# Kernel tuning notes

Hardware: AMD Instinct MI355X
Metric: run time of the kernel (lower is better)

The kernel has to match this reference:

```python
import jax, jax.numpy as jnp
import numpy as np

OBJ_DIM = 1024
NUM_REL_CLS = 8
N_OBJ = 4096
N_PAIRS = 65536


def setup_inputs() -> dict:
    key = jax.random.key(0)
    k1, k2, k3, k4, k5, k6 = jax.random.split(key, 6)
    obj_feats = jax.random.normal(k1, (N_OBJ, OBJ_DIM), dtype=jnp.float32)
    pairs = jax.random.randint(k2, (N_PAIRS, 2), 0, N_OBJ, dtype=jnp.int64)
    # proto_support_detector params: Linear(2*obj_dim -> obj_dim), Linear(obj_dim -> num_rel_cls)
    s1 = 1.0 / np.sqrt(2 * OBJ_DIM)
    s2 = 1.0 / np.sqrt(OBJ_DIM)
    W1 = jax.random.uniform(k3, (OBJ_DIM, 2 * OBJ_DIM), jnp.float32, -s1, s1)
    b1 = jax.random.uniform(k4, (OBJ_DIM,), jnp.float32, -s1, s1)
    W2 = jax.random.uniform(k5, (NUM_REL_CLS, OBJ_DIM), jnp.float32, -s2, s2)
    b2 = jax.random.uniform(k6, (NUM_REL_CLS,), jnp.float32, -s2, s2)
    return {"obj_feats": obj_feats, "pairs": pairs, "W1": W1, "b1": b1, "W2": W2, "b2": b2}


def reference(obj_feats, pairs, W1, b1, W2, b2):
    # Batched form of the per-pair proto_support_detector calls:
    #   rel_feat = Linear(cat([sub, obj], -1)); rel_dist = Linear(rel_feat)
    sub = obj_feats[pairs[:, 0]]                      # [P, D] gather
    obj = obj_feats[pairs[:, 1]]                      # [P, D] gather
    rel_feat = jnp.concatenate([sub, obj], axis=-1)   # [P, 2D]
    rel_feat = rel_feat @ W1.T + b1                   # [P, D]
    rel_dist = rel_feat @ W2.T + b2                   # [P, C]
    return rel_dist
```

## Files before the change

### kernel.cpp

```cpp
#include <hip/hip_runtime.h>

#define OBJ_DIM 1024
#define NREL 8
#define NOBJ 4096
#define NPAIRS 65536

#define WC_OFF   0
#define CVEC_OFF 16384
#define PROJ_OFF 16400

__global__ __launch_bounds__(256) void prep_kernel(
    const float* __restrict__ W1, const float* __restrict__ W2,
    const float* __restrict__ b1, float* __restrict__ Wc,
    float* __restrict__ cvec)
{
    const int cblk = blockIdx.x & 7;
    const int kblk = blockIdx.x >> 3;
    const int c  = cblk * 256 + threadIdx.x;
    const int k0 = kblk * 32;

    float acc[NREL];
#pragma unroll
    for (int r = 0; r < NREL; ++r) acc[r] = 0.f;

#pragma unroll 8
    for (int kk = 0; kk < 32; ++kk) {
        const int k = k0 + kk;
        const float w1 = W1[(size_t)k * 2048 + c];
#pragma unroll
        for (int r = 0; r < NREL; ++r)
            acc[r] += W2[r * 1024 + k] * w1;
    }
#pragma unroll
    for (int r = 0; r < NREL; ++r)
        atomicAdd(&Wc[r * 2048 + c], acc[r]);

    if (cblk == 0 && threadIdx.x < 32) {
        const int k = k0 + (int)threadIdx.x;
        const float bb = b1[k];
#pragma unroll
        for (int r = 0; r < NREL; ++r) {
            float v = W2[r * 1024 + k] * bb;
            v += __shfl_down(v, 16);
            v += __shfl_down(v, 8);
            v += __shfl_down(v, 4);
            v += __shfl_down(v, 2);
            v += __shfl_down(v, 1);
            if (threadIdx.x == 0) atomicAdd(&cvec[r], v);
        }
    }
}

__global__ __launch_bounds__(256) void proj_kernel(
    const float* __restrict__ obj, const float* __restrict__ Wc,
    float* __restrict__ proj)
{
    __shared__ float sh[16 * 1024];

    const int t = threadIdx.x;
#pragma unroll
    for (int i = 0; i < 16; ++i) {
        const int f4 = t + 256 * i;
        const int f  = f4 * 4;
        const int r   = f >> 11;
        const int rem = f & 2047;
        const int h   = rem >> 10;
        const int k   = rem & 1023;
        const float4 v = ((const float4*)Wc)[f4];
        *((float4*)&sh[(h * 8 + r) * 1024 + k]) = v;
    }
    __syncthreads();

    const int wave = t >> 6, lane = t & 63;
    const int n0 = blockIdx.x * 8 + wave * 2;
    const float4* xa = (const float4*)(obj + (size_t)n0 * 1024);
    const float4* xb = xa + 256;

    float4 x0[4], x1[4];
#pragma unroll
    for (int i = 0; i < 4; ++i) {
        x0[i] = xa[lane + 64 * i];
        x1[i] = xb[lane + 64 * i];
    }

    float a0[16], a1[16];
#pragma unroll
    for (int q = 0; q < 16; ++q) {
        float s0 = 0.f, s1 = 0.f;
        const float4* wq = (const float4*)(sh + q * 1024);
#pragma unroll
        for (int i = 0; i < 4; ++i) {
            const float4 w = wq[lane + 64 * i];
            s0 += w.x * x0[i].x + w.y * x0[i].y + w.z * x0[i].z + w.w * x0[i].w;
            s1 += w.x * x1[i].x + w.y * x1[i].y + w.z * x1[i].z + w.w * x1[i].w;
        }
        a0[q] = s0;
        a1[q] = s1;
    }
    __syncthreads();

    float* scr = sh + wave * 2304;
#pragma unroll
    for (int q4 = 0; q4 < 16; q4 += 4) {
        float4 w0 = make_float4(a0[q4], a0[q4 + 1], a0[q4 + 2], a0[q4 + 3]);
        float4 w1 = make_float4(a1[q4], a1[q4 + 1], a1[q4 + 2], a1[q4 + 3]);
        *((float4*)&scr[lane * 36 + q4])      = w0;
        *((float4*)&scr[lane * 36 + 16 + q4]) = w1;
    }
    __syncthreads();

    const int o = lane >> 1, half = lane & 1;
    float s = 0.f;
#pragma unroll 8
    for (int j = 0; j < 32; ++j)
        s += scr[(half * 32 + j) * 36 + o];
    s += __shfl_down(s, 1);
    if (half == 0) {
        const int row = o >> 4, q = o & 15;
        proj[(size_t)(n0 + row) * 16 + q] = s;
    }
}

__global__ __launch_bounds__(256) void gather_kernel(
    const int* __restrict__ pairs, const float* __restrict__ proj,
    const float* __restrict__ cvec, const float* __restrict__ b2,
    float* __restrict__ out)
{
    const int p = blockIdx.x * 256 + threadIdx.x;

    const int2 ij = ((const int2*)pairs)[p];

    const float4 c0 = ((const float4*)cvec)[0];
    const float4 c1 = ((const float4*)cvec)[1];
    const float4 d0 = ((const float4*)b2)[0];
    const float4 d1 = ((const float4*)b2)[1];

    const float4* ps = (const float4*)(proj + (size_t)ij.x * 16);
    const float4* po = (const float4*)(proj + (size_t)ij.y * 16 + 8);
    const float4 s0 = ps[0], s1 = ps[1];
    const float4 o0 = po[0], o1 = po[1];

    float4 r0, r1;
    r0.x = s0.x + o0.x + c0.x + d0.x;
    r0.y = s0.y + o0.y + c0.y + d0.y;
    r0.z = s0.z + o0.z + c0.z + d0.z;
    r0.w = s0.w + o0.w + c0.w + d0.w;
    r1.x = s1.x + o1.x + c1.x + d1.x;
    r1.y = s1.y + o1.y + c1.y + d1.y;
    r1.z = s1.z + o1.z + c1.z + d1.z;
    r1.w = s1.w + o1.w + c1.w + d1.w;

    ((float4*)out)[(size_t)p * 2]     = r0;
    ((float4*)out)[(size_t)p * 2 + 1] = r1;
}

extern "C" void kernel_launch(void* const* d_in, const int* in_sizes, int n_in,
                              void* d_out, int out_size, void* d_ws, size_t ws_size,
                              hipStream_t stream) {
    const float* obj   = (const float*)d_in[0];
    const int*   pairs = (const int*)d_in[1];
    const float* W1    = (const float*)d_in[2];
    const float* b1    = (const float*)d_in[3];
    const float* W2    = (const float*)d_in[4];
    const float* b2    = (const float*)d_in[5];
    float* out = (float*)d_out;

    float* ws   = (float*)d_ws;
    float* Wc   = ws + WC_OFF;
    float* cvec = ws + CVEC_OFF;
    float* proj = ws + PROJ_OFF;

    hipMemsetAsync(ws, 0, (size_t)(CVEC_OFF + 16) * sizeof(float), stream);

    prep_kernel<<<256, 256, 0, stream>>>(W1, W2, b1, Wc, cvec);
    proj_kernel<<<512, 256, 0, stream>>>(obj, Wc, proj);
    gather_kernel<<<NPAIRS / 256, 256, 0, stream>>>(pairs, proj, cvec, b2, out);
}
```

Before: 97.24 us.

## Fuse prep, projection and gather into one cooperative kernel with grid syncs

Merges the three kernels into a single cooperative launch of 256 blocks, separating the weight-combine, projection and pair-gather phases with grid-wide syncs. The aim is to remove the overhead and idle gaps of separate launches. The projection phase now handles four object rows per wave instead of two, so each block loads the combined weights into shared memory once for twice the rows. In exchange it adds grid-sync cost, more registers per thread, and only one block per CU in every phase. If the cooperative launch fails, it falls back to the original three-kernel path.

```diff
diff --git a/kernel.cpp b/kernel.cpp
--- a/kernel.cpp
+++ b/kernel.cpp
@@ -1,4 +1,7 @@
 #include <hip/hip_runtime.h>
+#include <hip/hip_cooperative_groups.h>
+
+namespace cg = cooperative_groups;
 
 #define OBJ_DIM 1024
 #define NREL 8
@@ -8,6 +11,162 @@
 #define WC_OFF   0
 #define CVEC_OFF 16384
 #define PROJ_OFF 16400
+
+__global__ __launch_bounds__(256) void fused_kernel(
+    const float* __restrict__ obj, const int* __restrict__ pairs,
+    const float* __restrict__ W1, const float* __restrict__ b1,
+    const float* __restrict__ W2, const float* __restrict__ b2,
+    float* __restrict__ ws, float* __restrict__ out)
+{
+    __shared__ float sh[16 * 1024];
+
+    float* Wc   = ws + WC_OFF;
+    float* cvec = ws + CVEC_OFF;
+    float* proj = ws + PROJ_OFF;
+
+    const int t = threadIdx.x;
+    const int b = blockIdx.x;
+    cg::grid_group grid = cg::this_grid();
+
+    {
+        const int cblk = b & 7;
+        const int kblk = b >> 3;
+        const int c  = cblk * 256 + t;
+        const int k0 = kblk * 32;
+
+        float acc[NREL];
+#pragma unroll
+        for (int r = 0; r < NREL; ++r) acc[r] = 0.f;
+
+#pragma unroll 8
+        for (int kk = 0; kk < 32; ++kk) {
+            const int k = k0 + kk;
+            const float w1 = W1[(size_t)k * 2048 + c];
+#pragma unroll
+            for (int r = 0; r < NREL; ++r)
+                acc[r] += W2[r * 1024 + k] * w1;
+        }
+#pragma unroll
+        for (int r = 0; r < NREL; ++r)
+            atomicAdd(&Wc[r * 2048 + c], acc[r]);
+
+        if (cblk == 0 && t < 32) {
+            const int k = k0 + t;
+            const float bb = b1[k];
+#pragma unroll
+            for (int r = 0; r < NREL; ++r) {
+                float v = W2[r * 1024 + k] * bb;
+                v += __shfl_down(v, 16);
+                v += __shfl_down(v, 8);
+                v += __shfl_down(v, 4);
+                v += __shfl_down(v, 2);
+                v += __shfl_down(v, 1);
+                if (t == 0) atomicAdd(&cvec[r], v);
+            }
+        }
+    }
+
+    grid.sync();
+
+    {
+#pragma unroll
+        for (int i = 0; i < 16; ++i) {
+            const int f4 = t + 256 * i;
+            const int f  = f4 * 4;
+            const int r   = f >> 11;
+            const int rem = f & 2047;
+            const int h   = rem >> 10;
+            const int k   = rem & 1023;
+            const float4 v = ((const float4*)Wc)[f4];
+            *((float4*)&sh[(h * 8 + r) * 1024 + k]) = v;
+        }
+        __syncthreads();
+
+        const int wave = t >> 6, lane = t & 63;
+        const int n0 = b * 16 + wave * 4;
+
+        float4 x[4][4];
+#pragma unroll
+        for (int r = 0; r < 4; ++r) {
+            const float4* xp = (const float4*)(obj + (size_t)(n0 + r) * 1024);
+#pragma unroll
+            for (int i = 0; i < 4; ++i) x[r][i] = xp[lane + 64 * i];
+        }
+
+        float a[4][16];
+#pragma unroll
+        for (int q = 0; q < 16; ++q) {
+            const float4* wq = (const float4*)(sh + q * 1024);
+            float s0 = 0.f, s1 = 0.f, s2 = 0.f, s3 = 0.f;
+#pragma unroll
+            for (int i = 0; i < 4; ++i) {
+                const float4 w = wq[lane + 64 * i];
+                s0 += w.x*x[0][i].x + w.y*x[0][i].y + w.z*x[0][i].z + w.w*x[0][i].w;
+                s1 += w.x*x[1][i].x + w.y*x[1][i].y + w.z*x[1][i].z + w.w*x[1][i].w;
+                s2 += w.x*x[2][i].x + w.y*x[2][i].y + w.z*x[2][i].z + w.w*x[2][i].w;
+                s3 += w.x*x[3][i].x + w.y*x[3][i].y + w.z*x[3][i].z + w.w*x[3][i].w;
+            }
+            a[0][q] = s0; a[1][q] = s1; a[2][q] = s2; a[3][q] = s3;
+        }
+        __syncthreads();
+
+        float* scr = sh + wave * 2304;
+#pragma unroll
+        for (int round = 0; round < 2; ++round) {
+#pragma unroll
+            for (int q4 = 0; q4 < 16; q4 += 4) {
+                *((float4*)&scr[lane * 36 + q4]) =
+                    make_float4(a[2*round][q4],   a[2*round][q4+1],
+                                a[2*round][q4+2], a[2*round][q4+3]);
+                *((float4*)&scr[lane * 36 + 16 + q4]) =
+                    make_float4(a[2*round+1][q4],   a[2*round+1][q4+1],
+                                a[2*round+1][q4+2], a[2*round+1][q4+3]);
+            }
+            __syncthreads();
+            const int o = lane >> 1, half = lane & 1;
+            float s = 0.f;
+#pragma unroll 8
+            for (int j = 0; j < 32; ++j)
+                s += scr[(half * 32 + j) * 36 + o];
+            s += __shfl_down(s, 1);
+            if (half == 0) {
+                const int row = 2 * round + (o >> 4), q = o & 15;
+                proj[(size_t)(n0 + row) * 16 + q] = s;
+            }
+            __syncthreads();
+        }
+    }
+
+    grid.sync();
+
+    {
+        const int p = b * 256 + t;
+        const int2 ij = ((const int2*)pairs)[p];
+
+        const float4 c0 = ((const float4*)cvec)[0];
+        const float4 c1 = ((const float4*)cvec)[1];
+        const float4 d0 = ((const float4*)b2)[0];
+        const float4 d1 = ((const float4*)b2)[1];
+
+        const float4* ps = (const float4*)(proj + (size_t)ij.x * 16);
+        const float4* po = (const float4*)(proj + (size_t)ij.y * 16 + 8);
+        const float4 s0 = ps[0], s1 = ps[1];
+        const float4 o0 = po[0], o1 = po[1];
+
+        float4 r0, r1;
+        r0.x = s0.x + o0.x + c0.x + d0.x;
+        r0.y = s0.y + o0.y + c0.y + d0.y;
+        r0.z = s0.z + o0.z + c0.z + d0.z;
+        r0.w = s0.w + o0.w + c0.w + d0.w;
+        r1.x = s1.x + o1.x + c1.x + d1.x;
+        r1.y = s1.y + o1.y + c1.y + d1.y;
+        r1.z = s1.z + o1.z + c1.z + d1.z;
+        r1.w = s1.w + o1.w + c1.w + d1.w;
+
+        ((float4*)out)[(size_t)p * 2]     = r0;
+        ((float4*)out)[(size_t)p * 2 + 1] = r1;
+    }
+}
 
 __global__ __launch_bounds__(256) void prep_kernel(
     const float* __restrict__ W1, const float* __restrict__ W2,
@@ -102,8 +261,8 @@
     float* scr = sh + wave * 2304;
 #pragma unroll
     for (int q4 = 0; q4 < 16; q4 += 4) {
-        float4 w0 = make_float4(a0[q4], a0[q4 + 1], a0[q4 + 2], a0[q4 + 3]);
-        float4 w1 = make_float4(a1[q4], a1[q4 + 1], a1[q4 + 2], a1[q4 + 3]);
+        float4 w0 = make_float4(a0[q4], a0[q4+1], a0[q4+2], a0[q4+3]);
+        float4 w1 = make_float4(a1[q4], a1[q4+1], a1[q4+2], a1[q4+3]);
         *((float4*)&scr[lane * 36 + q4])      = w0;
         *((float4*)&scr[lane * 36 + 16 + q4]) = w1;
     }
@@ -164,15 +323,21 @@
     const float* W2    = (const float*)d_in[4];
     const float* b2    = (const float*)d_in[5];
     float* out = (float*)d_out;
-
-    float* ws   = (float*)d_ws;
-    float* Wc   = ws + WC_OFF;
-    float* cvec = ws + CVEC_OFF;
-    float* proj = ws + PROJ_OFF;
+    float* ws  = (float*)d_ws;
 
     hipMemsetAsync(ws, 0, (size_t)(CVEC_OFF + 16) * sizeof(float), stream);
 
-    prep_kernel<<<256, 256, 0, stream>>>(W1, W2, b1, Wc, cvec);
-    proj_kernel<<<512, 256, 0, stream>>>(obj, Wc, proj);
-    gather_kernel<<<NPAIRS / 256, 256, 0, stream>>>(pairs, proj, cvec, b2, out);
-}
+    void* args[] = { (void*)&obj, (void*)&pairs, (void*)&W1, (void*)&b1,
+                     (void*)&W2, (void*)&b2, (void*)&ws, (void*)&out };
+    hipError_t err = hipLaunchCooperativeKernel((const void*)fused_kernel,
+                                                dim3(256), dim3(256), args,
+                                                0, stream);
+    if (err != hipSuccess) {
+        float* Wc   = ws + WC_OFF;
+        float* cvec = ws + CVEC_OFF;
+        float* proj = ws + PROJ_OFF;
+        prep_kernel<<<256, 256, 0, stream>>>(W1, W2, b1, Wc, cvec);
+        proj_kernel<<<512, 256, 0, stream>>>(obj, Wc, proj);
+        gather_kernel<<<NPAIRS / 256, 256, 0, stream>>>(pairs, proj, cvec, b2, out);
+    }
+}
```

Result: slower. 161.2 us (+65.8%).
